# Performance work log

Measured on AMD Instinct MI355X. Metric: run time of the kernel, lower is better.

## Reference

```python
import jax, jax.numpy as jnp
import numpy as np

B, N, D, H = 2, 4096, 512, 8
HD = D // H

def setup_inputs() -> dict:
    key = jax.random.key(0)
    ks = jax.random.split(key, 5)
    s = 1.0 / np.sqrt(D)
    return {
        "x": jax.random.normal(ks[0], (B, N, D), dtype=jnp.float32),
        "W_qkv": jax.random.uniform(ks[1], (D, 3 * D), minval=-s, maxval=s, dtype=jnp.float32),
        "b_qkv": jax.random.uniform(ks[2], (3 * D,), minval=-s, maxval=s, dtype=jnp.float32),
        "W_out": jax.random.uniform(ks[3], (D, D), minval=-s, maxval=s, dtype=jnp.float32),
        "b_out": jax.random.uniform(ks[4], (D,), minval=-s, maxval=s, dtype=jnp.float32),
    }

def reference(x, W_qkv, b_qkv, W_out, b_out):
    Bq, Nq, Dq = x.shape
    scale = HD ** -0.5
    qkv = x @ W_qkv + b_qkv                      # [B,N,3D]
    qkv = qkv.reshape(Bq, Nq, 3, H, HD)
    q, k, v = (jnp.moveaxis(qkv[:, :, i], 2, 1) for i in range(3))  # [B,H,N,hd]
    attn = jnp.einsum('bhqd,bhkd->bhqk', q, k) * scale   # [B,H,N,N]
    causal = jnp.tril(jnp.ones((Nq, Nq), dtype=bool))
    attn = jnp.where(causal, attn, -jnp.inf)
    attn = jax.nn.softmax(attn, axis=-1)
    out = jnp.einsum('bhqk,bhkd->bhqd', attn, v)         # [B,H,N,hd]
    out = jnp.moveaxis(out, 1, 2).reshape(Bq, Nq, Dq)
    return out @ W_out + b_out
```

## Files before the change

kernel.cpp:

```cpp
#include <hip/hip_runtime.h>
#include <hip/hip_bf16.h>


typedef __bf16 bf16_t;
typedef __bf16 bf16x2 __attribute__((ext_vector_type(2)));
typedef __bf16 bf16x4 __attribute__((ext_vector_type(4)));
typedef __bf16 bf16x8 __attribute__((ext_vector_type(8)));
typedef float  f32x4  __attribute__((ext_vector_type(4)));
typedef unsigned int uint32x4 __attribute__((ext_vector_type(4)));

__device__ __forceinline__ void gload_lds16(const bf16_t* g, bf16_t* l) {
    __builtin_amdgcn_global_load_lds(
        (const __attribute__((address_space(1))) void*)g,
        (__attribute__((address_space(3))) void*)l, 16, 0, 0);
}


__global__ void convert_f32_bf16(const float* __restrict__ in, bf16_t* __restrict__ out) {
    int i = blockIdx.x * 256 + threadIdx.x;
    float4 v = ((const float4*)in)[i];
    bf16x4 o;
    o[0] = (bf16_t)v.x; o[1] = (bf16_t)v.y; o[2] = (bf16_t)v.z; o[3] = (bf16_t)v.w;
    ((bf16x4*)out)[i] = o;
}

__global__ void transpose_tiled(const float* __restrict__ in, bf16_t* __restrict__ out, int N) {
    __shared__ bf16_t T[64][72];
    const int tid = threadIdx.x;
    const int n0 = blockIdx.x * 64, k0 = blockIdx.y * 64;
    #pragma unroll
    for (int pass = 0; pass < 4; ++pass) {
        int kk = pass * 16 + (tid >> 4), nn = (tid & 15) * 4;
        float4 v = *(const float4*)(in + (size_t)(k0 + kk) * N + n0 + nn);
        T[nn + 0][kk] = (bf16_t)v.x; T[nn + 1][kk] = (bf16_t)v.y;
        T[nn + 2][kk] = (bf16_t)v.z; T[nn + 3][kk] = (bf16_t)v.w;
    }
    __syncthreads();
    #pragma unroll
    for (int pass = 0; pass < 2; ++pass) {
        int n = pass * 32 + (tid >> 3), c8 = (tid & 7) * 8;
        *(bf16x8*)(out + (size_t)(n0 + n) * 512 + k0 + c8) = *(const bf16x8*)&T[n][c8];
    }
}

__global__ void transpose_v(const bf16_t* __restrict__ Vg, bf16_t* __restrict__ Vt) {
    __shared__ bf16_t T[64 * 64];
    const int tid = threadIdx.x;
    const int bh = blockIdx.x >> 6, n0 = (blockIdx.x & 63) * 64;
    const bf16_t* src = Vg + ((size_t)bh * 4096 + n0) * 64;
    #pragma unroll
    for (int i = 0; i < 2; ++i) {
        int c = tid + i * 256, n = c >> 3, h8 = (c & 7) * 8;
        bf16x8 v = *(const bf16x8*)(src + (size_t)n * 64 + h8);
        const int swz = (n >> 3) ^ (h8 >> 3);
        bf16_t* base = &T[swz * 8 + (n & 7)];
        #pragma unroll
        for (int j = 0; j < 8; ++j) base[(h8 + j) * 64] = v[j];
    }
    __syncthreads();
    bf16_t* dst = Vt + (size_t)bh * 64 * 4096 + n0;
    #pragma unroll
    for (int i = 0; i < 2; ++i) {
        int c = tid + i * 256, hd = c >> 3, cn = c & 7;
        *(bf16x8*)(dst + (size_t)hd * 4096 + cn * 8) =
            *(const bf16x8*)&T[hd * 64 + ((cn ^ (hd >> 3)) * 8)];
    }
}


template <int MODE, int TN>
__global__ __launch_bounds__(256) void gemm_bt(
    const bf16_t* __restrict__ A, const bf16_t* __restrict__ Bt,
    const float* __restrict__ bias,
    bf16_t* __restrict__ Qg, bf16_t* __restrict__ Kg, bf16_t* __restrict__ Vg,
    float* __restrict__ Cout)
{
    constexpr int NI = (TN == 128) ? 4 : 2;
    __shared__ bf16_t As[128 * 64];
    __shared__ bf16_t Bs[TN * 64];
    const int tid  = threadIdx.x;
    const int wid  = tid >> 6, lane = tid & 63, l16 = lane & 15, quad = lane >> 4;
    const int l8   = l16 & 7;
    const int wr   = (TN == 128) ? (wid >> 1) * 64 : wid * 32;
    const int wc   = (TN == 128) ? (wid & 1) * 64 : 0;
    const int m0   = blockIdx.y * 128, n0 = blockIdx.x * TN;

    f32x4 acc[NI][4] = {};

    for (int kk = 0; kk < 512; kk += 64) {
        __syncthreads();
        #pragma unroll
        for (int i = 0; i < 4; ++i) {
            int slot = tid + i * 256;
            int row = slot >> 3, cg = (slot & 7) ^ (row & 7);
            gload_lds16(A + (size_t)(m0 + row) * 512 + kk + cg * 8,
                        (bf16_t*)((char*)As + ((i * 256 + (wid << 6)) << 4)));
        }
        #pragma unroll
        for (int i = 0; i < TN / 32; ++i) {
            int slot = tid + i * 256;
            int row = slot >> 3, cg = (slot & 7) ^ (row & 7);
            gload_lds16(Bt + (size_t)(n0 + row) * 512 + kk + cg * 8,
                        (bf16_t*)((char*)Bs + ((i * 256 + (wid << 6)) << 4)));
        }
        __syncthreads();
        #pragma unroll
        for (int s = 0; s < 2; ++s) {
            const int sw = (s * 4 + quad);
            bf16x8 a[NI], b[4];
            #pragma unroll
            for (int i = 0; i < NI; ++i) {
                int row = wr + i * 16 + l16;
                a[i] = *(const bf16x8*)&As[(row * 8 + (sw ^ l8)) * 8];
            }
            #pragma unroll
            for (int j = 0; j < 4; ++j) {
                int row = wc + j * 16 + l16;
                b[j] = *(const bf16x8*)&Bs[(row * 8 + (sw ^ l8)) * 8];
            }
            #pragma unroll
            for (int i = 0; i < NI; ++i)
                #pragma unroll
                for (int j = 0; j < 4; ++j)
                    acc[i][j] = __builtin_amdgcn_mfma_f32_16x16x32_bf16(a[i], b[j], acc[i][j], 0, 0, 0);
        }
    }

    const float qscale = 0.18033688011112042f;
    #pragma unroll
    for (int i = 0; i < NI; ++i) {
        int mrow = m0 + wr + i * 16 + quad * 4;
        #pragma unroll
        for (int j = 0; j < 4; ++j) {
            int cgl = n0 + wc + j * 16 + l16;
            float bv = bias[cgl];
            #pragma unroll
            for (int r = 0; r < 4; ++r) {
                int m = mrow + r;
                float val = acc[i][j][r] + bv;
                if (MODE == 0) {
                    int which = cgl >> 9, hh = (cgl >> 6) & 7, hd = cgl & 63;
                    int b_ = m >> 12, n = m & 4095, bh = b_ * 8 + hh;
                    size_t idx = ((size_t)bh * 4096 + n) * 64 + hd;
                    if (which == 0)      Qg[idx] = (bf16_t)(val * qscale);
                    else if (which == 1) Kg[idx] = (bf16_t)val;
                    else                 Vg[idx] = (bf16_t)val;
                } else {
                    Cout[(size_t)m * 512 + cgl] = val;
                }
            }
        }
    }
}


__global__ __launch_bounds__(256, 3) void attn_ns2(
    const bf16_t* __restrict__ Qg, const bf16_t* __restrict__ Kg,
    const bf16_t* __restrict__ Vt,
    float* __restrict__ o_part, float* __restrict__ l_part, int nsplit)
{
    __shared__ bf16_t Ks[2][64][72];
    __shared__ bf16_t Vs[2][64][72];

    const int tid  = threadIdx.x;
    const int w    = tid >> 6, lane = tid & 63, l16 = lane & 15, quad = lane >> 4;
    const int bh   = blockIdx.x & 15, pr = (blockIdx.x >> 4) & 15, h = blockIdx.x >> 8;

    float* ob = o_part + (size_t)(h * 16 + bh) * 4096 * 64;
    float* lb = l_part + (size_t)(h * 16 + bh) * 4096;

    const int srow = tid >> 3, scol = (tid & 7) * 8;
    const int srow1 = srow + 32;
    const float MSHIFT = 12.0f;

    bf16x8 ones;
    #pragma unroll
    for (int j = 0; j < 8; ++j) ones[j] = (bf16_t)1.0f;

    uint4 kr0, kr1, vr0, vr1;

    for (int ph = 0; ph < 2; ++ph) {
        const int st = ph ? (31 - pr) : pr;
        const int T  = 2 * st + 2;
        const int b0 = (h * T) / nsplit, b1 = ((h + 1) * T) / nsplit;

        int qrow[2];
        bf16x8 qf[2][2];
        #pragma unroll
        for (int s = 0; s < 2; ++s) {
            qrow[s] = st * 128 + s * 64 + w * 16 + l16;
            const bf16_t* qp = Qg + ((size_t)bh * 4096 + qrow[s]) * 64;
            qf[s][0] = *(const bf16x8*)(qp + quad * 8);
            qf[s][1] = *(const bf16x8*)(qp + 32 + quad * 8);
        }

        f32x4 o[2][4] = {};
        f32x4 lacc[2] = {};

        {
            const size_t kb = ((size_t)bh * 4096 + b0 * 64) * 64;
            const size_t vb = (size_t)bh * 64 * 4096 + b0 * 64;
            kr0 = *(const uint4*)(Kg + kb + (size_t)srow * 64 + scol);
            kr1 = *(const uint4*)(Kg + kb + (size_t)srow1 * 64 + scol);
            vr0 = *(const uint4*)(Vt + vb + (size_t)srow * 4096 + scol);
            vr1 = *(const uint4*)(Vt + vb + (size_t)srow1 * 4096 + scol);
        }
        __syncthreads();

        for (int kt = b0; kt < b1; ++kt) {
            const int cur = kt & 1;
            *(uint4*)&Ks[cur][srow][scol]  = kr0;
            *(uint4*)&Ks[cur][srow1][scol] = kr1;
            *(uint4*)&Vs[cur][srow][scol]  = vr0;
            *(uint4*)&Vs[cur][srow1][scol] = vr1;
            __syncthreads();

            if (kt + 1 < b1) {
                const size_t kb = ((size_t)bh * 4096 + (kt + 1) * 64) * 64;
                const size_t vb = (size_t)bh * 64 * 4096 + (kt + 1) * 64;
                kr0 = *(const uint4*)(Kg + kb + (size_t)srow * 64 + scol);
                kr1 = *(const uint4*)(Kg + kb + (size_t)srow1 * 64 + scol);
                vr0 = *(const uint4*)(Vt + vb + (size_t)srow * 4096 + scol);
                vr1 = *(const uint4*)(Vt + vb + (size_t)srow1 * 4096 + scol);
            }

            bf16x8 kf[4][2], vf[4][2];
            #pragma unroll
            for (int cb = 0; cb < 4; ++cb) {
                kf[cb][0] = *(const bf16x8*)&Ks[cur][cb * 16 + l16][quad * 8];
                kf[cb][1] = *(const bf16x8*)&Ks[cur][cb * 16 + l16][32 + quad * 8];
            }
            #pragma unroll
            for (int j = 0; j < 4; ++j) {
                vf[j][0] = *(const bf16x8*)&Vs[cur][j * 16 + l16][quad * 8];
                vf[j][1] = *(const bf16x8*)&Vs[cur][j * 16 + l16][32 + quad * 8];
            }

            #pragma unroll
            for (int s = 0; s < 2; ++s) {
                const int diag = 2 * st + s;
                if (kt > diag) continue;

                f32x4 sv[4] = {};
                #pragma unroll
                for (int cb = 0; cb < 4; ++cb) {
                    sv[cb] = __builtin_amdgcn_mfma_f32_16x16x32_bf16(kf[cb][0], qf[s][0], sv[cb], 0, 0, 0);
                    sv[cb] = __builtin_amdgcn_mfma_f32_16x16x32_bf16(kf[cb][1], qf[s][1], sv[cb], 0, 0, 0);
                }

                if (kt == diag) {
                    #pragma unroll
                    for (int cb = 0; cb < 4; ++cb) {
                        const int keyg = kt * 64 + cb * 16 + quad * 4;
                        #pragma unroll
                        for (int r = 0; r < 4; ++r)
                            if (keyg + r > qrow[s]) sv[cb][r] = -1e30f;
                    }
                }

                unsigned int c[4][2];
                #pragma unroll
                for (int cb = 0; cb < 4; ++cb) {
                    #pragma unroll
                    for (int t = 0; t < 2; ++t) {
                        bf16x2 pk2;
                        pk2[0] = (bf16_t)__builtin_amdgcn_exp2f(sv[cb][2 * t]     - MSHIFT);
                        pk2[1] = (bf16_t)__builtin_amdgcn_exp2f(sv[cb][2 * t + 1] - MSHIFT);
                        c[cb][t] = __builtin_bit_cast(unsigned int, pk2);
                    }
                }

                unsigned int pw0[4], pw1[4];
                #pragma unroll
                for (int t = 0; t < 2; ++t) {
                    auto u  = __builtin_amdgcn_permlane32_swap(c[0][t], c[1][t], false, false);
                    auto z  = __builtin_amdgcn_permlane16_swap(u[0], u[1], false, false);
                    pw0[t] = z[0]; pw0[t + 2] = z[1];
                    auto u2 = __builtin_amdgcn_permlane32_swap(c[2][t], c[3][t], false, false);
                    auto z2 = __builtin_amdgcn_permlane16_swap(u2[0], u2[1], false, false);
                    pw1[t] = z2[0]; pw1[t + 2] = z2[1];
                }
                uint32x4 w0v = {pw0[0], pw0[1], pw0[2], pw0[3]};
                uint32x4 w1v = {pw1[0], pw1[1], pw1[2], pw1[3]};
                bf16x8 pa0 = __builtin_bit_cast(bf16x8, w0v);
                bf16x8 pa1 = __builtin_bit_cast(bf16x8, w1v);

                #pragma unroll
                for (int j = 0; j < 4; ++j) {
                    o[s][j] = __builtin_amdgcn_mfma_f32_16x16x32_bf16(pa0, vf[j][0], o[s][j], 0, 0, 0);
                    o[s][j] = __builtin_amdgcn_mfma_f32_16x16x32_bf16(pa1, vf[j][1], o[s][j], 0, 0, 0);
                }
                lacc[s] = __builtin_amdgcn_mfma_f32_16x16x32_bf16(pa0, ones, lacc[s], 0, 0, 0);
                lacc[s] = __builtin_amdgcn_mfma_f32_16x16x32_bf16(pa1, ones, lacc[s], 0, 0, 0);
            }
        }

        #pragma unroll
        for (int s = 0; s < 2; ++s)
            #pragma unroll
            for (int r = 0; r < 4; ++r) {
                int n = st * 128 + s * 64 + w * 16 + quad * 4 + r;
                #pragma unroll
                for (int j = 0; j < 4; ++j)
                    ob[(size_t)n * 64 + j * 16 + l16] = o[s][j][r];
                if (l16 == 0) lb[n] = lacc[s][r];
            }
    }
}

__global__ void combine_kernel(const float* __restrict__ o_part,
                               const float* __restrict__ l_part,
                               bf16_t* __restrict__ Og, int ns)
{
    int t = blockIdx.x * 256 + threadIdx.x;
    int oct = t & 7, n = (t >> 3) & 4095, bh = t >> 15;
    size_t base = ((size_t)bh * 4096 + n) * 64 + oct * 8;
    f32x4 s0 = {}, s1 = {};
    float l = 0.f;
    for (int h = 0; h < ns; ++h) {
        const float* op = o_part + (size_t)h * 16 * 4096 * 64 + base;
        s0 += *(const f32x4*)op;
        s1 += *(const f32x4*)(op + 4);
        l  += l_part[(size_t)h * 16 * 4096 + (size_t)bh * 4096 + n];
    }
    float inv = 1.0f / l;
    bf16x8 res;
    #pragma unroll
    for (int j = 0; j < 4; ++j) {
        res[j]     = (bf16_t)(s0[j] * inv);
        res[j + 4] = (bf16_t)(s1[j] * inv);
    }
    *(bf16x8*)(Og + ((size_t)((bh >> 3) * 4096 + n)) * 512 + (bh & 7) * 64 + oct * 8) = res;
}


extern "C" void kernel_launch(void* const* d_in, const int* in_sizes, int n_in,
                              void* d_out, int out_size, void* d_ws, size_t ws_size,
                              hipStream_t stream) {
    const float* x    = (const float*)d_in[0];
    const float* Wqkv = (const float*)d_in[1];
    const float* bqkv = (const float*)d_in[2];
    const float* Wout = (const float*)d_in[3];
    const float* bout = (const float*)d_in[4];
    float* out = (float*)d_out;

    char* ws = (char*)d_ws;
    bf16_t* xb  = (bf16_t*)(ws);
    bf16_t* WqT = (bf16_t*)(ws + 8388608);
    bf16_t* WoT = (bf16_t*)(ws + 9961472);
    bf16_t* Qg  = (bf16_t*)(ws + 10485760);
    bf16_t* Kg  = (bf16_t*)(ws + 18874368);
    bf16_t* Vt  = (bf16_t*)(ws + 27262976);
    bf16_t* Vg  = (bf16_t*)(ws + 35651584);

    const int nsplit = (ws_size >= 103809024ULL) ? 4
                     : (ws_size >= 86769664ULL)  ? 3 : 2;
    float* o_part = (float*)(ws + 35651584);
    float* l_part = (float*)(ws + 35651584 + (size_t)nsplit * 16777216);

    convert_f32_bf16<<<4096, 256, 0, stream>>>(x, xb);
    transpose_tiled<<<dim3(24, 8), 256, 0, stream>>>(Wqkv, WqT, 1536);
    transpose_tiled<<<dim3(8, 8), 256, 0, stream>>>(Wout, WoT, 512);

    gemm_bt<0, 128><<<dim3(12, 64), 256, 0, stream>>>(xb, WqT, bqkv, Qg, Kg, Vg, nullptr);
    transpose_v<<<1024, 256, 0, stream>>>(Vg, Vt);

    attn_ns2<<<256 * nsplit, 256, 0, stream>>>(Qg, Kg, Vt, o_part, l_part, nsplit);
    combine_kernel<<<2048, 256, 0, stream>>>(o_part, l_part, xb , nsplit);

    gemm_bt<1, 64><<<dim3(8, 64), 256, 0, stream>>>(xb, WoT, bout, nullptr, nullptr, nullptr, out);
}
```

Baseline: 187.3 us.

## Load K/V fragments directly from global memory, dropping LDS staging

The attention kernel no longer stages K and V tiles through double-buffered shared memory with register prefetch and block barriers. Each wave now reads its MFMA fragments straight from global memory, relying on L1/L2 caching, since all four waves read the same tile. This removes LDS traffic and the __syncthreads per tile, and frees shared memory for occupancy. The cost is four times the global/cache load traffic and exposed load latency without explicit prefetch.

```diff
diff --git a/kernel.cpp b/kernel.cpp
--- a/kernel.cpp
+++ b/kernel.cpp
@@ -159,9 +159,6 @@
     const bf16_t* __restrict__ Vt,
     float* __restrict__ o_part, float* __restrict__ l_part, int nsplit)
 {
-    __shared__ bf16_t Ks[2][64][72];
-    __shared__ bf16_t Vs[2][64][72];
-
     const int tid  = threadIdx.x;
     const int w    = tid >> 6, lane = tid & 63, l16 = lane & 15, quad = lane >> 4;
     const int bh   = blockIdx.x & 15, pr = (blockIdx.x >> 4) & 15, h = blockIdx.x >> 8;
@@ -169,15 +166,14 @@
     float* ob = o_part + (size_t)(h * 16 + bh) * 4096 * 64;
     float* lb = l_part + (size_t)(h * 16 + bh) * 4096;
 
-    const int srow = tid >> 3, scol = (tid & 7) * 8;
-    const int srow1 = srow + 32;
     const float MSHIFT = 12.0f;
 
     bf16x8 ones;
     #pragma unroll
     for (int j = 0; j < 8; ++j) ones[j] = (bf16_t)1.0f;
 
-    uint4 kr0, kr1, vr0, vr1;
+    const bf16_t* kbase = Kg + (size_t)bh * 262144 + (size_t)l16 * 64 + quad * 8;
+    const bf16_t* vbase = Vt + (size_t)bh * 262144 + (size_t)l16 * 4096 + quad * 8;
 
     for (int ph = 0; ph < 2; ++ph) {
         const int st = ph ? (31 - pr) : pr;
@@ -197,43 +193,20 @@
         f32x4 o[2][4] = {};
         f32x4 lacc[2] = {};
 
-        {
-            const size_t kb = ((size_t)bh * 4096 + b0 * 64) * 64;
-            const size_t vb = (size_t)bh * 64 * 4096 + b0 * 64;
-            kr0 = *(const uint4*)(Kg + kb + (size_t)srow * 64 + scol);
-            kr1 = *(const uint4*)(Kg + kb + (size_t)srow1 * 64 + scol);
-            vr0 = *(const uint4*)(Vt + vb + (size_t)srow * 4096 + scol);
-            vr1 = *(const uint4*)(Vt + vb + (size_t)srow1 * 4096 + scol);
-        }
-        __syncthreads();
-
         for (int kt = b0; kt < b1; ++kt) {
-            const int cur = kt & 1;
-            *(uint4*)&Ks[cur][srow][scol]  = kr0;
-            *(uint4*)&Ks[cur][srow1][scol] = kr1;
-            *(uint4*)&Vs[cur][srow][scol]  = vr0;
-            *(uint4*)&Vs[cur][srow1][scol] = vr1;
-            __syncthreads();
-
-            if (kt + 1 < b1) {
-                const size_t kb = ((size_t)bh * 4096 + (kt + 1) * 64) * 64;
-                const size_t vb = (size_t)bh * 64 * 4096 + (kt + 1) * 64;
-                kr0 = *(const uint4*)(Kg + kb + (size_t)srow * 64 + scol);
-                kr1 = *(const uint4*)(Kg + kb + (size_t)srow1 * 64 + scol);
-                vr0 = *(const uint4*)(Vt + vb + (size_t)srow * 4096 + scol);
-                vr1 = *(const uint4*)(Vt + vb + (size_t)srow1 * 4096 + scol);
-            }
+            const bf16_t* kp = kbase + (size_t)kt * 4096;
+            const bf16_t* vp = vbase + (size_t)kt * 64;
 
             bf16x8 kf[4][2], vf[4][2];
             #pragma unroll
             for (int cb = 0; cb < 4; ++cb) {
-                kf[cb][0] = *(const bf16x8*)&Ks[cur][cb * 16 + l16][quad * 8];
-                kf[cb][1] = *(const bf16x8*)&Ks[cur][cb * 16 + l16][32 + quad * 8];
+                kf[cb][0] = *(const bf16x8*)(kp + cb * 1024);
+                kf[cb][1] = *(const bf16x8*)(kp + cb * 1024 + 32);
             }
             #pragma unroll
             for (int j = 0; j < 4; ++j) {
-                vf[j][0] = *(const bf16x8*)&Vs[cur][j * 16 + l16][quad * 8];
-                vf[j][1] = *(const bf16x8*)&Vs[cur][j * 16 + l16][32 + quad * 8];
+                vf[j][0] = *(const bf16x8*)(vp + (size_t)j * 65536);
+                vf[j][1] = *(const bf16x8*)(vp + (size_t)j * 65536 + 32);
             }
 
             #pragma unroll
```

New measurement: 259.2 us. 38.4% more time.
